# Kernel tuning notes

Hardware: AMD Instinct MI355X
Metric: run time of the kernel (lower is better)

The kernel has to match this reference:

```python
import jax, jax.numpy as jnp
import numpy as np

B, S, D = 1, 2048, 2048
HQ, HKV = 32, 8
HD = D // HQ          # 64
G = HQ // HKV         # 4 query heads per kv head


def apply_rope(x, freq):
    # x: (b, h, s, hd); freq: (s, hd//2) angles. Llama-style pairwise rotation.
    cos = jnp.cos(freq)  # (s, hd//2)
    sin = jnp.sin(freq)
    xr = x.reshape(*x.shape[:-1], HD // 2, 2)
    xe, xo = xr[..., 0], xr[..., 1]
    re = xe * cos - xo * sin
    ro = xe * sin + xo * cos
    return jnp.stack([re, ro], axis=-1).reshape(x.shape)


def setup_inputs() -> dict:
    key = jax.random.key(0)
    k1, k2, k3, k4, k5 = jax.random.split(key, 5)
    x = jax.random.normal(k1, (B, S, D), dtype=jnp.float32)
    # RoPE angles: pos * inv_freq, theta=10000
    inv_freq = 1.0 / (10000.0 ** (jnp.arange(0, HD, 2, dtype=jnp.float32) / HD))
    freq = jnp.arange(S, dtype=jnp.float32)[:, None] * inv_freq[None, :]  # (S, HD//2)
    mask = jnp.tril(jnp.ones((S, S), dtype=jnp.int32))
    scale = D ** -0.5
    wq = jax.random.normal(k2, (D, HQ * HD), dtype=jnp.float32) * scale
    wk = jax.random.normal(k3, (D, HKV * HD), dtype=jnp.float32) * scale
    wv = jax.random.normal(k4, (D, HKV * HD), dtype=jnp.float32) * scale
    wo = jax.random.normal(k5, (HQ * HD, D), dtype=jnp.float32) * scale
    return {"x": x, "freq": freq, "mask": mask, "wq": wq, "wk": wk, "wv": wv, "wo": wo}


def reference(x, freq, mask, wq, wk, wv, wo):
    b, s, d = x.shape
    q = (x @ wq).reshape(b, s, HQ, HD).transpose(0, 2, 1, 3)    # (b,HQ,s,hd)
    k = (x @ wk).reshape(b, s, HKV, HD).transpose(0, 2, 1, 3)   # (b,HKV,s,hd)
    v = (x @ wv).reshape(b, s, HKV, HD).transpose(0, 2, 1, 3)
    q = apply_rope(q, freq[:s])
    k = apply_rope(k, freq[:s])
    # GQA: broadcast kv heads over groups instead of repeat_interleave
    qg = q.reshape(b, HKV, G, s, HD)
    scores = jnp.einsum('bhgsd,bhtd->bhgst', qg, k)             # (b,HKV,G,s,s)
    scores = jnp.where(mask[:s, :s] == 0, -jnp.inf, scores)
    w = jax.nn.softmax(scores * (HD ** -0.5), axis=-1)
    out = jnp.einsum('bhgst,bhtd->bhgsd', w, v)
    out = out.reshape(b, HQ, s, HD).transpose(0, 2, 1, 3).reshape(b, s, HQ * HD)
    return out @ wo
```

## Files before the change

### kernel.cpp

```cpp
#include <hip/hip_runtime.h>

typedef unsigned short u16;
typedef unsigned int u32;
typedef unsigned long long u64;

using bf16x8 = __bf16 __attribute__((ext_vector_type(8)));
using f32x4  = float  __attribute__((ext_vector_type(4)));

#define LDS_SPACE __attribute__((address_space(3)))
#define GLB_SPACE __attribute__((address_space(1)))

static __device__ __forceinline__ u16 f2bf(float f) {
  union { float f; u32 u; } c; c.f = f;
  u32 u = c.u;
  return (u16)((u + 0x7fffu + ((u >> 16) & 1u)) >> 16);
}
static __device__ __forceinline__ float bf2f(u16 u) {
  union { u32 u; float f; } c; c.u = ((u32)u) << 16;
  return c.f;
}

static __device__ __forceinline__ void fence_barrier() {
  asm volatile("" ::: "memory");
  __builtin_amdgcn_s_barrier();
  asm volatile("" ::: "memory");
}

constexpr float SC = 0.18033688011112042f;

__global__ __launch_bounds__(256) void prep_k(const float* __restrict__ x,
                                              const float* __restrict__ wq,
                                              const float* __restrict__ wk,
                                              const float* __restrict__ wv,
                                              const float* __restrict__ wo,
                                              u16* __restrict__ x_bf,
                                              u16* __restrict__ wqkv_t,
                                              u16* __restrict__ wo_t) {
  const int b = blockIdx.x;
  if (b < 4096) {
    int i = b * 256 + threadIdx.x;
    float4 v = ((const float4*)x)[i];
    ushort4 o;
    o.x = f2bf(v.x); o.y = f2bf(v.y); o.z = f2bf(v.z); o.w = f2bf(v.w);
    ((ushort4*)x_bf)[i] = o;
    return;
  }
  const float* src; u16* dst; int C, bx, by; float scale = 1.0f;
  if (b < 8192)      { src = wq; dst = wqkv_t; C = 2048; int t = b - 4096; bx = t & 63; by = t >> 6; scale = SC; }
  else if (b < 9216) { src = wk; dst = wqkv_t + (size_t)2048 * 2048; C = 512; int t = b - 8192; bx = t & 15; by = t >> 4; }
  else if (b < 10240){ src = wv; dst = wqkv_t + (size_t)2560 * 2048; C = 512; int t = b - 9216; bx = t & 15; by = t >> 4; }
  else               { src = wo; dst = wo_t; C = 2048; int t = b - 10240; bx = t & 63; by = t >> 6; }
  __shared__ float t[32][33];
  const int lx = threadIdx.x & 31, ly = threadIdx.x >> 5;
  const int r0 = by * 32, c0 = bx * 32;
  #pragma unroll
  for (int i = 0; i < 32; i += 8)
    t[ly + i][lx] = src[(size_t)(r0 + ly + i) * C + c0 + lx];
  __syncthreads();
  #pragma unroll
  for (int i = 0; i < 32; i += 8)
    dst[(size_t)(c0 + ly + i) * 2048 + r0 + lx] = f2bf(t[lx][ly + i] * scale);
}

__global__ __launch_bounds__(256) void vtrans_k(const u16* __restrict__ Y,
                                                u16* __restrict__ Vt) {
  __shared__ u16 t[64][72];
  const int s0 = blockIdx.x * 64;
  const int c0 = blockIdx.y * 64;
  const int lx = threadIdx.x & 63, ly = threadIdx.x >> 6;
  #pragma unroll
  for (int i = 0; i < 64; i += 4)
    t[i + ly][lx] = Y[(size_t)(s0 + i + ly) * 3072 + 2560 + c0 + lx];
  __syncthreads();
  #pragma unroll
  for (int i = 0; i < 64; i += 4)
    Vt[(size_t)(c0 + i + ly) * 2048 + s0 + lx] = t[lx][i + ly];
}

template <typename OutT, int BN>
__global__ __launch_bounds__(256) void gemm64_k(const u16* __restrict__ A,
                                                const u16* __restrict__ Bt,
                                                OutT* __restrict__ C,
                                                int M, int N, int K) {
  constexpr int WN = BN / 32;
  __shared__ u16 As[2][64 * 64];
  __shared__ u16 Bs[2][BN * 64];
  const int tid = threadIdx.x, lane = tid & 63, w = tid >> 6;
  const int wr = w >> 1, wc = w & 1;
  const int bm = blockIdx.y, bn = blockIdx.x;
  const int l15 = lane & 15, lq = lane >> 4;
  f32x4 acc[2][WN] = {};

  const int srow8 = lane >> 3;
  const int scolb = ((lane & 7) ^ srow8) * 16;
  const u16* AgR = A + (size_t)(bm * 64 + w * 16 + srow8) * K;
  const u16* BgR = Bt + (size_t)(bn * BN + w * (BN / 4) + srow8) * K;

  auto stage = [&](int buf, int k0) {
    #pragma unroll
    for (int i = 0; i < 2; ++i)
      __builtin_amdgcn_global_load_lds(
          (const GLB_SPACE u32*)((const char*)(AgR + (size_t)i * 8 * K + k0) + scolb),
          (LDS_SPACE u32*)&As[buf][(w * 16 + i * 8) * 64], 16, 0, 0);
    #pragma unroll
    for (int i = 0; i < WN; ++i)
      __builtin_amdgcn_global_load_lds(
          (const GLB_SPACE u32*)((const char*)(BgR + (size_t)i * 8 * K + k0) + scolb),
          (LDS_SPACE u32*)&Bs[buf][(w * (BN / 4) + i * 8) * 64], 16, 0, 0);
  };

  stage(0, 0);
  for (int k0 = 0; k0 < K; k0 += 64) {
    const int cur = (k0 >> 6) & 1;
    fence_barrier();
    if (k0 + 64 < K) {
      stage(cur ^ 1, k0 + 64);
      if constexpr (BN == 128) asm volatile("s_waitcnt vmcnt(6)" ::: "memory");
      else                     asm volatile("s_waitcnt vmcnt(4)" ::: "memory");
    } else {
      asm volatile("s_waitcnt vmcnt(0)" ::: "memory");
    }
    fence_barrier();

    #pragma unroll
    for (int kk = 0; kk < 2; ++kk) {
      bf16x8 a[2], b[WN];
      #pragma unroll
      for (int m = 0; m < 2; ++m) {
        const int ra = wr * 32 + m * 16 + l15;
        a[m] = *(const bf16x8*)&As[cur][ra * 64 + (((kk * 4 + lq) ^ (ra & 7)) << 3)];
      }
      #pragma unroll
      for (int n = 0; n < WN; ++n) {
        const int rb = wc * (BN / 2) + n * 16 + l15;
        b[n] = *(const bf16x8*)&Bs[cur][rb * 64 + (((kk * 4 + lq) ^ (rb & 7)) << 3)];
      }
      #pragma unroll
      for (int m = 0; m < 2; ++m)
        #pragma unroll
        for (int n = 0; n < WN; ++n)
          acc[m][n] = __builtin_amdgcn_mfma_f32_16x16x32_bf16(a[m], b[n], acc[m][n], 0, 0, 0);
    }
  }

  const int r0 = bm * 64 + wr * 32 + lq * 4;
  const int c0 = bn * BN + wc * (BN / 2) + l15;
  #pragma unroll
  for (int m = 0; m < 2; ++m)
    #pragma unroll
    for (int n = 0; n < WN; ++n)
      #pragma unroll
      for (int r = 0; r < 4; ++r) {
        float v = acc[m][n][r];
        size_t off = (size_t)(r0 + m * 16 + r) * N + (c0 + n * 16);
        if constexpr (sizeof(OutT) == 2) ((u16*)C)[off] = f2bf(v);
        else C[off] = v;
      }
}

__global__ __launch_bounds__(256) void rope_k(u16* __restrict__ Y,
                                              const float* __restrict__ freq) {
  int idx = blockIdx.x * 256 + threadIdx.x;
  int s = idx / 1280;
  int rem = idx - s * 1280;
  int h = rem >> 5;
  int i = rem & 31;
  int col = (h < 32) ? (h * 64 + 2 * i) : (2048 + (h - 32) * 64 + 2 * i);
  float ang = freq[s * 32 + i];
  float sn, cs;
  sincosf(ang, &sn, &cs);
  size_t base = (size_t)s * 3072 + col;
  float e = bf2f(Y[base]), o = bf2f(Y[base + 1]);
  Y[base]     = f2bf(e * cs - o * sn);
  Y[base + 1] = f2bf(e * sn + o * cs);
}

__global__ __launch_bounds__(256, 3) void attn_part_k(const u16* __restrict__ Y,
                                                      const u16* __restrict__ Vtg,
                                                      u16* __restrict__ Opart,
                                                      float2* __restrict__ Ml,
                                                      u16* __restrict__ Out) {
  __shared__ u16 Ks[2][64 * 64];
  __shared__ u16 Vs[2][64 * 64];
  __shared__ u32 Ps[4][16 * 32];
  const int w = threadIdx.x >> 6, lane = threadIdx.x & 63;
  const int l15 = lane & 15, lq = lane >> 4;

  const int b = (int)blockIdx.x;
  const int head = b & 31;
  const int idx = b >> 5;
  const u64 tb = (idx < 12) ? 986161012810415591ULL : 1200400570313029ULL;
  const int v = (int)((tb >> ((idx < 12 ? idx : idx - 12) * 5)) & 31);
  const int qt = v & 15, ch = v >> 4;
  const int kvh = head >> 2;
  const int ntiles = 2 * qt + 2;
  const int half = qt + 1;
  const int tstart = ch ? half : 0;
  const int tend = (qt >= 8 && ch == 0) ? half : ntiles;
  const int q0w = qt * 128 + w * 32;

  const int srow = lane >> 3;
  const int scolb = ((lane & 7) ^ srow) * 16;
  auto stage = [&](int buf, int t) {
    const int t0 = t * 64;
    #pragma unroll
    for (int i = 0; i < 2; ++i) {
      const int r = w * 16 + i * 8;
      const char* gk = (const char*)(Y + (size_t)(t0 + r + srow) * 3072 + 2048 + kvh * 64) + scolb;
      __builtin_amdgcn_global_load_lds((const GLB_SPACE u32*)gk,
                                       (LDS_SPACE u32*)&Ks[buf][r * 64], 16, 0, 0);
      const char* gv = (const char*)(Vtg + (size_t)(kvh * 64 + r + srow) * 2048 + t0) + scolb;
      __builtin_amdgcn_global_load_lds((const GLB_SPACE u32*)gv,
                                       (LDS_SPACE u32*)&Vs[buf][r * 64], 16, 0, 0);
    }
  };

  stage(0, tstart);

  bf16x8 qf[2][2];
  #pragma unroll
  for (int qs = 0; qs < 2; ++qs)
    #pragma unroll
    for (int kk = 0; kk < 2; ++kk)
      qf[qs][kk] = *(const bf16x8*)&Y[(size_t)(q0w + qs * 16 + l15) * 3072 +
                                      head * 64 + kk * 32 + lq * 8];

  float m_[2] = { -1e30f, -1e30f };
  float l_[2] = { 0.f, 0.f };
  f32x4 accO[2][4] = {};

  for (int t = tstart; t < tend; ++t) {
    const int cur = (t - tstart) & 1;
    fence_barrier();
    if (t + 1 < tend) {
      stage(cur ^ 1, t + 1);
      asm volatile("s_waitcnt vmcnt(4)" ::: "memory");
    } else {
      asm volatile("s_waitcnt vmcnt(0)" ::: "memory");
    }
    fence_barrier();

    const int t0 = t * 64;
    if (t0 > q0w + 31) continue;

    const u16* Kb = Ks[cur];
    const u16* Vb = Vs[cur];

    f32x4 sc[2][4] = {};
    #pragma unroll
    for (int kk = 0; kk < 2; ++kk)
      #pragma unroll
      for (int kt = 0; kt < 4; ++kt) {
        const int rk = kt * 16 + l15;
        bf16x8 a = *(const bf16x8*)&Kb[rk * 64 + ((((kk * 4 + lq) ^ (rk & 7)) << 3))];
        sc[0][kt] = __builtin_amdgcn_mfma_f32_16x16x32_bf16(a, qf[0][kk], sc[0][kt], 0, 0, 0);
        sc[1][kt] = __builtin_amdgcn_mfma_f32_16x16x32_bf16(a, qf[1][kk], sc[1][kt], 0, 0, 0);
      }

    bf16x8 vf[2][4];
    #pragma unroll
    for (int c = 0; c < 2; ++c)
      #pragma unroll
      for (int dt = 0; dt < 4; ++dt) {
        const int rv = dt * 16 + l15;
        vf[c][dt] = *(const bf16x8*)&Vb[rv * 64 + ((((c * 4 + lq) ^ (rv & 7)) << 3))];
      }

    #pragma unroll
    for (int qs = 0; qs < 2; ++qs) {
      const int qsmin = q0w + qs * 16;
      if (t0 > qsmin + 15) continue;
      const int qrow = qsmin + l15;
      if (t0 + 63 > qsmin) {
        #pragma unroll
        for (int n = 0; n < 4; ++n)
          #pragma unroll
          for (int rr = 0; rr < 4; ++rr)
            if (t0 + n * 16 + lq * 4 + rr > qrow) sc[qs][n][rr] = -1e30f;
      }
      float a0 = fmaxf(fmaxf(sc[qs][0][0], sc[qs][0][1]), fmaxf(sc[qs][0][2], sc[qs][0][3]));
      float a1 = fmaxf(fmaxf(sc[qs][1][0], sc[qs][1][1]), fmaxf(sc[qs][1][2], sc[qs][1][3]));
      float a2 = fmaxf(fmaxf(sc[qs][2][0], sc[qs][2][1]), fmaxf(sc[qs][2][2], sc[qs][2][3]));
      float a3 = fmaxf(fmaxf(sc[qs][3][0], sc[qs][3][1]), fmaxf(sc[qs][3][2], sc[qs][3][3]));
      float mx = fmaxf(fmaxf(a0, a1), fmaxf(a2, a3));

      if (__any(mx > m_[qs] + 7.25f)) {
        float mf = mx;
        mf = fmaxf(mf, __shfl_xor(mf, 16));
        mf = fmaxf(mf, __shfl_xor(mf, 32));
        const float mnew = fmaxf(m_[qs], mf);
        const float alpha = exp2f(m_[qs] - mnew);
        l_[qs] *= alpha;
        #pragma unroll
        for (int dt = 0; dt < 4; ++dt) accO[qs][dt] *= alpha;
        m_[qs] = mnew;
      }
      const float mS = m_[qs];
      float s0 = 0.f, s1 = 0.f, s2 = 0.f, s3 = 0.f;
      #pragma unroll
      for (int n = 0; n < 4; ++n) {
        float p0 = exp2f(sc[qs][n][0] - mS);
        float p1 = exp2f(sc[qs][n][1] - mS);
        float p2 = exp2f(sc[qs][n][2] - mS);
        float p3 = exp2f(sc[qs][n][3] - mS);
        s0 += p0; s1 += p1; s2 += p2; s3 += p3;
        u32 w0, w1;
        asm("v_cvt_pk_bf16_f32 %0, %1, %2" : "=v"(w0) : "v"(p0), "v"(p1));
        asm("v_cvt_pk_bf16_f32 %0, %1, %2" : "=v"(w1) : "v"(p2), "v"(p3));
        const u32 pidx = l15 * 32 + ((lq * 2 + n * 8) ^ ((l15 & 7) << 2));
        *(u64*)&Ps[w][pidx] = (u64)w0 | ((u64)w1 << 32);
      }
      l_[qs] += (s0 + s1) + (s2 + s3);

      const u16* p16 = (const u16*)Ps[w];
      #pragma unroll
      for (int c = 0; c < 2; ++c) {
        bf16x8 bb = *(const bf16x8*)&p16[l15 * 64 + ((c * 32 + lq * 8) ^ ((l15 & 7) << 3))];
        #pragma unroll
        for (int dt = 0; dt < 4; ++dt)
          accO[qs][dt] = __builtin_amdgcn_mfma_f32_16x16x32_bf16(vf[c][dt], bb, accO[qs][dt], 0, 0, 0);
      }
    }
  }

  if (qt < 8) {
    #pragma unroll
    for (int qs = 0; qs < 2; ++qs) {
      float lt = l_[qs];
      lt += __shfl_xor(lt, 16);
      lt += __shfl_xor(lt, 32);
      const float rl = 1.0f / lt;
      const int qrow = q0w + qs * 16 + l15;
      #pragma unroll
      for (int dt = 0; dt < 4; ++dt) {
        ushort4 o;
        o.x = f2bf(accO[qs][dt][0] * rl);
        o.y = f2bf(accO[qs][dt][1] * rl);
        o.z = f2bf(accO[qs][dt][2] * rl);
        o.w = f2bf(accO[qs][dt][3] * rl);
        *(ushort4*)&Out[(size_t)qrow * 2048 + head * 64 + dt * 16 + lq * 4] = o;
      }
    }
    return;
  }

  const int slot = ((head << 3) + (qt - 8)) * 2 + ch;
  u16* ob = Opart + (size_t)slot * 8192;
  #pragma unroll
  for (int qs = 0; qs < 2; ++qs) {
    float lt = l_[qs];
    lt += __shfl_xor(lt, 16);
    lt += __shfl_xor(lt, 32);
    const int row = w * 32 + qs * 16 + l15;
    #pragma unroll
    for (int dt = 0; dt < 4; ++dt) {
      ushort4 o;
      o.x = f2bf(accO[qs][dt][0]);
      o.y = f2bf(accO[qs][dt][1]);
      o.z = f2bf(accO[qs][dt][2]);
      o.w = f2bf(accO[qs][dt][3]);
      *(ushort4*)&ob[row * 64 + dt * 16 + lq * 4] = o;
    }
    if (lq == 0) Ml[(size_t)slot * 128 + row] = make_float2(m_[qs], lt);
  }
}

__global__ __launch_bounds__(256) void attn_comb_k(const u16* __restrict__ Opart,
                                                   const float2* __restrict__ Ml,
                                                   u16* __restrict__ Out) {
  const int b = blockIdx.x;
  const int rg = b & 3;
  const int hq = b >> 2;
  const int head = hq >> 3;
  const int qt8 = hq & 7;
  const int slot0 = ((head << 3) + qt8) * 2;
  const int rl = threadIdx.x >> 3;
  const int d8 = (threadIdx.x & 7) * 8;
  const int row = rg * 32 + rl;

  float2 ml0 = Ml[(size_t)slot0 * 128 + row];
  float2 ml1 = Ml[(size_t)(slot0 + 1) * 128 + row];
  const float gm = fmaxf(ml0.x, ml1.x);
  const float a0 = exp2f(ml0.x - gm);
  const float a1 = exp2f(ml1.x - gm);
  const float rd = 1.0f / (a0 * ml0.y + a1 * ml1.y);

  const u16* p0 = &Opart[(size_t)slot0 * 8192 + row * 64 + d8];
  const u16* p1 = &Opart[(size_t)(slot0 + 1) * 8192 + row * 64 + d8];
  ushort4 q0 = *(const ushort4*)p0, q1 = *(const ushort4*)(p0 + 4);
  ushort4 r0 = *(const ushort4*)p1, r1 = *(const ushort4*)(p1 + 4);
  ushort4 o0, o1;
  o0.x = f2bf((a0 * bf2f(q0.x) + a1 * bf2f(r0.x)) * rd);
  o0.y = f2bf((a0 * bf2f(q0.y) + a1 * bf2f(r0.y)) * rd);
  o0.z = f2bf((a0 * bf2f(q0.z) + a1 * bf2f(r0.z)) * rd);
  o0.w = f2bf((a0 * bf2f(q0.w) + a1 * bf2f(r0.w)) * rd);
  o1.x = f2bf((a0 * bf2f(q1.x) + a1 * bf2f(r1.x)) * rd);
  o1.y = f2bf((a0 * bf2f(q1.y) + a1 * bf2f(r1.y)) * rd);
  o1.z = f2bf((a0 * bf2f(q1.z) + a1 * bf2f(r1.z)) * rd);
  o1.w = f2bf((a0 * bf2f(q1.w) + a1 * bf2f(r1.w)) * rd);
  u16* op = &Out[(size_t)((qt8 + 8) * 128 + row) * 2048 + head * 64 + d8];
  *(ushort4*)op = o0;
  *(ushort4*)(op + 4) = o1;
}

extern "C" void kernel_launch(void* const* d_in, const int* in_sizes, int n_in,
                              void* d_out, int out_size, void* d_ws, size_t ws_size,
                              hipStream_t stream) {
  const float* x    = (const float*)d_in[0];
  const float* freq = (const float*)d_in[1];
  const float* wq   = (const float*)d_in[3];
  const float* wk   = (const float*)d_in[4];
  const float* wv   = (const float*)d_in[5];
  const float* wo   = (const float*)d_in[6];
  float* out = (float*)d_out;

  u16* x_bf   = (u16*)d_ws;
  u16* wqkv_t = x_bf + (size_t)2048 * 2048;
  u16* wo_t   = wqkv_t + (size_t)3072 * 2048;
  u16* y      = wo_t + (size_t)2048 * 2048;
  u16* attn   = y + (size_t)2048 * 3072;
  u16* vt     = x_bf;
  u16* opart  = attn + (size_t)2048 * 2048;
  float2* ml  = (float2*)(opart + (size_t)512 * 8192);

  prep_k<<<14336, 256, 0, stream>>>(x, wq, wk, wv, wo, x_bf, wqkv_t, wo_t);
  gemm64_k<u16, 128><<<dim3(24, 32), 256, 0, stream>>>(x_bf, wqkv_t, y, 2048, 3072, 2048);
  rope_k<<<10240, 256, 0, stream>>>(y, freq);
  vtrans_k<<<dim3(32, 8), 256, 0, stream>>>(y, vt);
  attn_part_k<<<768, 256, 0, stream>>>(y, vt, opart, ml, attn);
  attn_comb_k<<<1024, 256, 0, stream>>>(opart, ml, attn);
  gemm64_k<float, 64><<<dim3(32, 32), 256, 0, stream>>>(attn, wo_t, out, 2048, 2048, 2048);
}
```

Baseline: 135.1 us.

## Restructure GEMM and attention double-buffering to one barrier per iteration

Both the GEMM and attention loops now issue the next tile's global-to-LDS prefetch at the top of the iteration, compute on the current buffer, then wait for all loads and barrier once at the end. This replaces the two barriers and partial vmcnt waits per iteration. The attention kernel also precomputes per-lane LDS byte offsets and global base pointers so the inner loop does less address math. In exchange, every iteration waits for the whole prefetch with vmcnt(0), and the attention loop issues a redundant stage on its last iteration.

```diff
diff --git a/kernel.cpp b/kernel.cpp
--- a/kernel.cpp
+++ b/kernel.cpp
@@ -110,17 +110,12 @@
   };
 
   stage(0, 0);
+  asm volatile("s_waitcnt vmcnt(0)" ::: "memory");
+  fence_barrier();
+
   for (int k0 = 0; k0 < K; k0 += 64) {
-    const int cur = (k0 >> 6) & 1;
-    fence_barrier();
-    if (k0 + 64 < K) {
-      stage(cur ^ 1, k0 + 64);
-      if constexpr (BN == 128) asm volatile("s_waitcnt vmcnt(6)" ::: "memory");
-      else                     asm volatile("s_waitcnt vmcnt(4)" ::: "memory");
-    } else {
-      asm volatile("s_waitcnt vmcnt(0)" ::: "memory");
-    }
-    fence_barrier();
+    const int p = (k0 >> 6) & 1;
+    if (k0 + 64 < K) stage(p ^ 1, k0 + 64);
 
     #pragma unroll
     for (int kk = 0; kk < 2; ++kk) {
@@ -128,12 +123,12 @@
       #pragma unroll
       for (int m = 0; m < 2; ++m) {
         const int ra = wr * 32 + m * 16 + l15;
-        a[m] = *(const bf16x8*)&As[cur][ra * 64 + (((kk * 4 + lq) ^ (ra & 7)) << 3)];
+        a[m] = *(const bf16x8*)&As[p][ra * 64 + (((kk * 4 + lq) ^ (ra & 7)) << 3)];
       }
       #pragma unroll
       for (int n = 0; n < WN; ++n) {
         const int rb = wc * (BN / 2) + n * 16 + l15;
-        b[n] = *(const bf16x8*)&Bs[cur][rb * 64 + (((kk * 4 + lq) ^ (rb & 7)) << 3)];
+        b[n] = *(const bf16x8*)&Bs[p][rb * 64 + (((kk * 4 + lq) ^ (rb & 7)) << 3)];
       }
       #pragma unroll
       for (int m = 0; m < 2; ++m)
@@ -141,6 +136,9 @@
         for (int n = 0; n < WN; ++n)
           acc[m][n] = __builtin_amdgcn_mfma_f32_16x16x32_bf16(a[m], b[n], acc[m][n], 0, 0, 0);
     }
+
+    asm volatile("s_waitcnt vmcnt(0)" ::: "memory");
+    fence_barrier();
   }
 
   const int r0 = bm * 64 + wr * 32 + lq * 4;
@@ -201,21 +199,31 @@
 
   const int srow = lane >> 3;
   const int scolb = ((lane & 7) ^ srow) * 16;
+  const char* gkB = (const char*)(Y + (size_t)(w * 16 + srow) * 3072 + 2048 + kvh * 64) + scolb;
+  const char* gvB = (const char*)(Vtg + (size_t)(kvh * 64 + w * 16 + srow) * 2048) + scolb;
+
   auto stage = [&](int buf, int t) {
-    const int t0 = t * 64;
+    const size_t t0 = (size_t)t * 64;
     #pragma unroll
     for (int i = 0; i < 2; ++i) {
-      const int r = w * 16 + i * 8;
-      const char* gk = (const char*)(Y + (size_t)(t0 + r + srow) * 3072 + 2048 + kvh * 64) + scolb;
-      __builtin_amdgcn_global_load_lds((const GLB_SPACE u32*)gk,
-                                       (LDS_SPACE u32*)&Ks[buf][r * 64], 16, 0, 0);
-      const char* gv = (const char*)(Vtg + (size_t)(kvh * 64 + r + srow) * 2048 + t0) + scolb;
-      __builtin_amdgcn_global_load_lds((const GLB_SPACE u32*)gv,
-                                       (LDS_SPACE u32*)&Vs[buf][r * 64], 16, 0, 0);
+      __builtin_amdgcn_global_load_lds((const GLB_SPACE u32*)(gkB + t0 * 6144 + (size_t)i * 49152),
+                                       (LDS_SPACE u32*)&Ks[buf][(w * 16 + i * 8) * 64], 16, 0, 0);
+      __builtin_amdgcn_global_load_lds((const GLB_SPACE u32*)(gvB + t0 * 2 + (size_t)i * 32768),
+                                       (LDS_SPACE u32*)&Vs[buf][(w * 16 + i * 8) * 64], 16, 0, 0);
     }
   };
 
-  stage(0, tstart);
+  int rowB[4], xk[2], pwr[4], prd[2];
+  #pragma unroll
+  for (int kt = 0; kt < 4; ++kt) rowB[kt] = (kt * 16 + l15) * 128;
+  #pragma unroll
+  for (int kk = 0; kk < 2; ++kk) xk[kk] = (((kk * 4 + lq) ^ (l15 & 7)) << 4);
+  #pragma unroll
+  for (int n = 0; n < 4; ++n)
+    pwr[n] = (l15 * 32 + ((lq * 2 + n * 8) ^ ((l15 & 7) << 2))) * 4;
+  #pragma unroll
+  for (int c = 0; c < 2; ++c)
+    prd[c] = l15 * 128 + (((c * 32 + lq * 8) ^ ((l15 & 7) << 3)) << 1);
 
   bf16x8 qf[2][2];
   #pragma unroll
@@ -229,98 +237,94 @@
   float l_[2] = { 0.f, 0.f };
   f32x4 accO[2][4] = {};
 
+  stage(0, tstart);
+  asm volatile("s_waitcnt vmcnt(0)" ::: "memory");
+  fence_barrier();
+
   for (int t = tstart; t < tend; ++t) {
-    const int cur = (t - tstart) & 1;
-    fence_barrier();
-    if (t + 1 < tend) {
-      stage(cur ^ 1, t + 1);
-      asm volatile("s_waitcnt vmcnt(4)" ::: "memory");
-    } else {
-      asm volatile("s_waitcnt vmcnt(0)" ::: "memory");
-    }
-    fence_barrier();
+    const int p = (t - tstart) & 1;
+    stage(p ^ 1, (t + 1 < tend) ? t + 1 : t);
 
     const int t0 = t * 64;
-    if (t0 > q0w + 31) continue;
-
-    const u16* Kb = Ks[cur];
-    const u16* Vb = Vs[cur];
-
-    f32x4 sc[2][4] = {};
-    #pragma unroll
-    for (int kk = 0; kk < 2; ++kk)
-      #pragma unroll
-      for (int kt = 0; kt < 4; ++kt) {
-        const int rk = kt * 16 + l15;
-        bf16x8 a = *(const bf16x8*)&Kb[rk * 64 + ((((kk * 4 + lq) ^ (rk & 7)) << 3))];
-        sc[0][kt] = __builtin_amdgcn_mfma_f32_16x16x32_bf16(a, qf[0][kk], sc[0][kt], 0, 0, 0);
-        sc[1][kt] = __builtin_amdgcn_mfma_f32_16x16x32_bf16(a, qf[1][kk], sc[1][kt], 0, 0, 0);
-      }
-
-    bf16x8 vf[2][4];
-    #pragma unroll
-    for (int c = 0; c < 2; ++c)
-      #pragma unroll
-      for (int dt = 0; dt < 4; ++dt) {
-        const int rv = dt * 16 + l15;
-        vf[c][dt] = *(const bf16x8*)&Vb[rv * 64 + ((((c * 4 + lq) ^ (rv & 7)) << 3))];
-      }
-
-    #pragma unroll
-    for (int qs = 0; qs < 2; ++qs) {
-      const int qsmin = q0w + qs * 16;
-      if (t0 > qsmin + 15) continue;
-      const int qrow = qsmin + l15;
-      if (t0 + 63 > qsmin) {
+    if (t0 <= q0w + 31) {
+      const char* KbC = (const char*)Ks[p];
+      const char* VbC = (const char*)Vs[p];
+
+      f32x4 sc[2][4] = {};
+      #pragma unroll
+      for (int kk = 0; kk < 2; ++kk)
         #pragma unroll
-        for (int n = 0; n < 4; ++n)
-          #pragma unroll
-          for (int rr = 0; rr < 4; ++rr)
-            if (t0 + n * 16 + lq * 4 + rr > qrow) sc[qs][n][rr] = -1e30f;
-      }
-      float a0 = fmaxf(fmaxf(sc[qs][0][0], sc[qs][0][1]), fmaxf(sc[qs][0][2], sc[qs][0][3]));
-      float a1 = fmaxf(fmaxf(sc[qs][1][0], sc[qs][1][1]), fmaxf(sc[qs][1][2], sc[qs][1][3]));
-      float a2 = fmaxf(fmaxf(sc[qs][2][0], sc[qs][2][1]), fmaxf(sc[qs][2][2], sc[qs][2][3]));
-      float a3 = fmaxf(fmaxf(sc[qs][3][0], sc[qs][3][1]), fmaxf(sc[qs][3][2], sc[qs][3][3]));
-      float mx = fmaxf(fmaxf(a0, a1), fmaxf(a2, a3));
-
-      if (__any(mx > m_[qs] + 7.25f)) {
-        float mf = mx;
-        mf = fmaxf(mf, __shfl_xor(mf, 16));
-        mf = fmaxf(mf, __shfl_xor(mf, 32));
-        const float mnew = fmaxf(m_[qs], mf);
-        const float alpha = exp2f(m_[qs] - mnew);
-        l_[qs] *= alpha;
-        #pragma unroll
-        for (int dt = 0; dt < 4; ++dt) accO[qs][dt] *= alpha;
-        m_[qs] = mnew;
-      }
-      const float mS = m_[qs];
-      float s0 = 0.f, s1 = 0.f, s2 = 0.f, s3 = 0.f;
-      #pragma unroll
-      for (int n = 0; n < 4; ++n) {
-        float p0 = exp2f(sc[qs][n][0] - mS);
-        float p1 = exp2f(sc[qs][n][1] - mS);
-        float p2 = exp2f(sc[qs][n][2] - mS);
-        float p3 = exp2f(sc[qs][n][3] - mS);
-        s0 += p0; s1 += p1; s2 += p2; s3 += p3;
-        u32 w0, w1;
-        asm("v_cvt_pk_bf16_f32 %0, %1, %2" : "=v"(w0) : "v"(p0), "v"(p1));
-        asm("v_cvt_pk_bf16_f32 %0, %1, %2" : "=v"(w1) : "v"(p2), "v"(p3));
-        const u32 pidx = l15 * 32 + ((lq * 2 + n * 8) ^ ((l15 & 7) << 2));
-        *(u64*)&Ps[w][pidx] = (u64)w0 | ((u64)w1 << 32);
-      }
-      l_[qs] += (s0 + s1) + (s2 + s3);
-
-      const u16* p16 = (const u16*)Ps[w];
-      #pragma unroll
-      for (int c = 0; c < 2; ++c) {
-        bf16x8 bb = *(const bf16x8*)&p16[l15 * 64 + ((c * 32 + lq * 8) ^ ((l15 & 7) << 3))];
+        for (int kt = 0; kt < 4; ++kt) {
+          bf16x8 a = *(const bf16x8*)(KbC + rowB[kt] + xk[kk]);
+          sc[0][kt] = __builtin_amdgcn_mfma_f32_16x16x32_bf16(a, qf[0][kk], sc[0][kt], 0, 0, 0);
+          sc[1][kt] = __builtin_amdgcn_mfma_f32_16x16x32_bf16(a, qf[1][kk], sc[1][kt], 0, 0, 0);
+        }
+
+      bf16x8 vf[2][4];
+      #pragma unroll
+      for (int c = 0; c < 2; ++c)
         #pragma unroll
         for (int dt = 0; dt < 4; ++dt)
-          accO[qs][dt] = __builtin_amdgcn_mfma_f32_16x16x32_bf16(vf[c][dt], bb, accO[qs][dt], 0, 0, 0);
+          vf[c][dt] = *(const bf16x8*)(VbC + rowB[dt] + xk[c]);
+
+      #pragma unroll
+      for (int qs = 0; qs < 2; ++qs) {
+        const int qsmin = q0w + qs * 16;
+        if (t0 > qsmin + 15) continue;
+        const int qrow = qsmin + l15;
+        if (t0 + 63 > qsmin) {
+          #pragma unroll
+          for (int n = 0; n < 4; ++n)
+            #pragma unroll
+            for (int rr = 0; rr < 4; ++rr)
+              if (t0 + n * 16 + lq * 4 + rr > qrow) sc[qs][n][rr] = -1e30f;
+        }
+        float a0 = fmaxf(fmaxf(sc[qs][0][0], sc[qs][0][1]), fmaxf(sc[qs][0][2], sc[qs][0][3]));
+        float a1 = fmaxf(fmaxf(sc[qs][1][0], sc[qs][1][1]), fmaxf(sc[qs][1][2], sc[qs][1][3]));
+        float a2 = fmaxf(fmaxf(sc[qs][2][0], sc[qs][2][1]), fmaxf(sc[qs][2][2], sc[qs][2][3]));
+        float a3 = fmaxf(fmaxf(sc[qs][3][0], sc[qs][3][1]), fmaxf(sc[qs][3][2], sc[qs][3][3]));
+        float mx = fmaxf(fmaxf(a0, a1), fmaxf(a2, a3));
+
+        if (__any(mx > m_[qs] + 7.25f)) {
+          float mf = mx;
+          mf = fmaxf(mf, __shfl_xor(mf, 16));
+          mf = fmaxf(mf, __shfl_xor(mf, 32));
+          const float mnew = fmaxf(m_[qs], mf);
+          const float alpha = exp2f(m_[qs] - mnew);
+          l_[qs] *= alpha;
+          #pragma unroll
+          for (int dt = 0; dt < 4; ++dt) accO[qs][dt] *= alpha;
+          m_[qs] = mnew;
+        }
+        const float mS = m_[qs];
+        float s0 = 0.f, s1 = 0.f, s2 = 0.f, s3 = 0.f;
+        char* psB = (char*)Ps[w];
+        #pragma unroll
+        for (int n = 0; n < 4; ++n) {
+          float p0 = exp2f(sc[qs][n][0] - mS);
+          float p1 = exp2f(sc[qs][n][1] - mS);
+          float p2 = exp2f(sc[qs][n][2] - mS);
+          float p3 = exp2f(sc[qs][n][3] - mS);
+          s0 += p0; s1 += p1; s2 += p2; s3 += p3;
+          u32 w0, w1;
+          asm("v_cvt_pk_bf16_f32 %0, %1, %2" : "=v"(w0) : "v"(p0), "v"(p1));
+          asm("v_cvt_pk_bf16_f32 %0, %1, %2" : "=v"(w1) : "v"(p2), "v"(p3));
+          *(u64*)(psB + pwr[n]) = (u64)w0 | ((u64)w1 << 32);
+        }
+        l_[qs] += (s0 + s1) + (s2 + s3);
+
+        #pragma unroll
+        for (int c = 0; c < 2; ++c) {
+          bf16x8 bb = *(const bf16x8*)(psB + prd[c]);
+          #pragma unroll
+          for (int dt = 0; dt < 4; ++dt)
+            accO[qs][dt] = __builtin_amdgcn_mfma_f32_16x16x32_bf16(vf[c][dt], bb, accO[qs][dt], 0, 0, 0);
+        }
       }
     }
+
+    asm volatile("s_waitcnt vmcnt(0)" ::: "memory");
+    fence_barrier();
   }
 
   if (qt < 8) {
```

After: 135.8 us. About the same (+0.6%).
